# Kernel tuning notes

Measured on AMD Instinct MI355X. Metric: run time of the kernel, lower is better.

The kernel has to match this reference:

```python
import jax, jax.numpy as jnp
import numpy as np

STRIDES = (8, 16, 32)
NC = 80            # num_classes
BINS = 16          # dfl_bins
TOPK = 10          # tal_topk
TAL_ALPHA, TAL_BETA = 0.5, 6.0   # ultralytics TaskAlignedAssigner defaults
EPS = 1e-9
FOCAL_A, FOCAL_G = 0.25, 2.0
W_CLS, W_IOU, W_DFL = 0.5, 7.5, 1.5


def _make_grid(H, W, stride):
    ys, xs = jnp.meshgrid(jnp.arange(H, dtype=jnp.float32), jnp.arange(W, dtype=jnp.float32), indexing='ij')
    return jnp.stack([(xs + 0.5) * stride, (ys + 0.5) * stride], -1).reshape(H * W, 2)


def _flatten(p):
    # (B,C,H,W) -> cls (B,N,NC), dfl (B,N,4,BINS); channel layout = [4*BINS dfl | NC cls]
    B, C, H, W = p.shape
    p = p.transpose(0, 2, 3, 1).reshape(B, H * W, C)
    return p[..., 4 * BINS:], p[..., :4 * BINS].reshape(B, H * W, 4, BINS)


def _pairwise_iou(gt, pr):
    # gt (B,G,4), pr (B,N,4) -> iou (B,G,N)
    g = gt[:, :, None]
    p = pr[:, None]
    lt = jnp.maximum(g[..., :2], p[..., :2])
    rb = jnp.minimum(g[..., 2:], p[..., 2:])
    wh = jnp.clip(rb - lt, 0.0)
    inter = wh[..., 0] * wh[..., 1]
    ag = (g[..., 2] - g[..., 0]) * (g[..., 3] - g[..., 1])
    ap = jnp.clip(p[..., 2] - p[..., 0], 0.0) * jnp.clip(p[..., 3] - p[..., 1], 0.0)
    return inter / (ag + ap - inter + EPS)


def _ciou_loss(p, t):
    # elementwise CIoU loss, (...,4) xyxy -> (...)
    px1, py1, px2, py2 = p[..., 0], p[..., 1], p[..., 2], p[..., 3]
    tx1, ty1, tx2, ty2 = t[..., 0], t[..., 1], t[..., 2], t[..., 3]
    w1, h1 = px2 - px1, py2 - py1
    w2, h2 = tx2 - tx1, ty2 - ty1
    inter = jnp.clip(jnp.minimum(px2, tx2) - jnp.maximum(px1, tx1), 0.0) * \
            jnp.clip(jnp.minimum(py2, ty2) - jnp.maximum(py1, ty1), 0.0)
    union = w1 * h1 + w2 * h2 - inter + EPS
    iou = inter / union
    cw = jnp.maximum(px2, tx2) - jnp.minimum(px1, tx1)
    ch = jnp.maximum(py2, ty2) - jnp.minimum(py1, ty1)
    c2 = cw * cw + ch * ch + EPS
    rho2 = ((px1 + px2 - tx1 - tx2) ** 2 + (py1 + py2 - ty1 - ty2) ** 2) / 4.0
    v = (4.0 / np.pi ** 2) * (jnp.arctan(w2 / (h2 + EPS)) - jnp.arctan(w1 / (h1 + EPS))) ** 2
    alpha = jax.lax.stop_gradient(v / (v - iou + (1.0 + EPS)))
    return 1.0 - (iou - rho2 / c2 - v * alpha)


def _tal_assign(cls_prob, pred_boxes, grids, gt_bboxes, gt_labels):
    B, N, C = cls_prob.shape
    G = gt_bboxes.shape[1]
    idx = jnp.broadcast_to(gt_labels[:, None, :], (B, N, G))
    scores = jnp.take_along_axis(cls_prob, idx, axis=2).transpose(0, 2, 1)  # (B,G,N)
    overlaps = _pairwise_iou(gt_bboxes, pred_boxes)                          # (B,G,N)
    align = scores ** TAL_ALPHA * overlaps ** TAL_BETA
    x, y = grids[:, 0], grids[:, 1]
    in_gts = ((x[None, None] > gt_bboxes[..., 0:1]) & (x[None, None] < gt_bboxes[..., 2:3]) &
              (y[None, None] > gt_bboxes[..., 1:2]) & (y[None, None] < gt_bboxes[..., 3:4]))
    metric = jnp.where(in_gts, align, 0.0)
    vals, idxs = jax.lax.top_k(metric, TOPK)                                 # (B,G,TOPK)
    bi = jnp.arange(B)[:, None, None]
    gi = jnp.arange(G)[None, :, None]
    topk_mask = jnp.zeros((B, G, N), bool).at[bi, gi, idxs].set(vals > EPS)
    mask_pos = topk_mask & in_gts
    multi = mask_pos.sum(1) > 1                                              # (B,N)
    is_max = jnp.argmax(overlaps, 1)[:, None, :] == jnp.arange(G)[None, :, None]
    mask_pos = jnp.where(multi[:, None, :], is_max, mask_pos)
    fg = mask_pos.any(1)                                                     # (B,N)
    matched = jnp.argmax(mask_pos, 1)                                        # (B,N)
    mi = jnp.where(fg, matched, -1)
    b2 = jnp.arange(B)[:, None]
    tb = gt_bboxes[b2, matched]                                              # (B,N,4)
    tl = gt_labels[b2, matched]                                              # (B,N)
    mpf = mask_pos.astype(align.dtype)
    align_m = align * mpf
    ov_m = overlaps * mpf
    norm = (align_m * ov_m.max(-1, keepdims=True) / (align_m.max(-1, keepdims=True) + EPS)).max(1)
    ts = jax.nn.one_hot(tl, C, dtype=align.dtype) * norm[..., None] * fg[..., None]
    return ts, tb, fg, mi


def _dfl_targets(gt_bboxes, mi, fgf, grids, stride_map):
    # vectorized version of _make_dfl_targets: soft two-bin scatter per coord
    B, N = mi.shape
    b2 = jnp.arange(B)[:, None]
    boxes = gt_bboxes[b2, jnp.maximum(mi, 0)]                                # (B,N,4)
    cx, cy = grids[:, 0], grids[:, 1]
    d = jnp.stack([jnp.clip(cx - boxes[..., 0], 0.0), jnp.clip(cy - boxes[..., 1], 0.0),
                   jnp.clip(boxes[..., 2] - cx, 0.0), jnp.clip(boxes[..., 3] - cy, 0.0)], -1)
    d = jnp.clip(d / stride_map[None, :, None], 0.0, BINS - 1 - 1e-6)
    lo = jnp.floor(d)
    a = d - lo
    lo_i = lo.astype(jnp.int32)
    up_i = jnp.minimum(lo_i + 1, BINS - 1)
    td = jax.nn.one_hot(lo_i, BINS) * (1.0 - a)[..., None] + jax.nn.one_hot(up_i, BINS) * a[..., None]
    return td * fgf[..., None, None]                                         # (B,N,4,BINS)


def _focal_sum(logits, targets):
    logits = logits.reshape(-1, NC)
    targets = targets.reshape(-1, NC)
    p = jax.nn.sigmoid(logits)
    # stable BCE-with-logits
    ce = jnp.maximum(logits, 0.0) - logits * targets + jnp.log1p(jnp.exp(-jnp.abs(logits)))
    p_t = p * targets + (1.0 - p) * (1.0 - targets)
    a_t = targets * FOCAL_A + (1.0 - targets) * (1.0 - FOCAL_A)
    return (a_t * (1.0 - p_t) ** FOCAL_G * ce).sum()


def _loss(p0, p1, p2, gt_bboxes, gt_labels):
    cls_l, dfl_l, grid_l, str_l = [], [], [], []
    for p, s in zip((p0, p1, p2), STRIDES):
        c, d = _flatten(p)
        cls_l.append(c)
        dfl_l.append(d)
        H, W = p.shape[2], p.shape[3]
        grid_l.append(_make_grid(H, W, s))
        str_l.append(jnp.full((H * W,), float(s), jnp.float32))
    all_cls = jnp.concatenate(cls_l, 1)       # (B,N,NC)
    all_dfl = jnp.concatenate(dfl_l, 1)       # (B,N,4,BINS)
    grids = jnp.concatenate(grid_l, 0)        # (N,2)
    stride_map = jnp.concatenate(str_l, 0)    # (N,)
    # DFL decode: expectation over bins * stride -> ltrb -> xyxy
    dist = (jax.nn.softmax(all_dfl, -1) * jnp.arange(BINS, dtype=jnp.float32)).sum(-1) * stride_map[None, :, None]
    cx, cy = grids[:, 0], grids[:, 1]
    pred_boxes = jnp.stack([cx - dist[..., 0], cy - dist[..., 1], cx + dist[..., 2], cy + dist[..., 3]], -1)
    # assignment under stop_gradient (torch.no_grad in the original)
    cls_prob = jax.lax.stop_gradient(jax.nn.sigmoid(all_cls))
    pb_sg = jax.lax.stop_gradient(pred_boxes)
    ts, tb, fg, mi = _tal_assign(cls_prob, pb_sg, grids, gt_bboxes, gt_labels)
    ts = jax.lax.stop_gradient(ts)
    tb = jax.lax.stop_gradient(tb)
    fgf = fg.astype(jnp.float32)
    den = jnp.maximum(fg.sum(), 1).astype(jnp.float32)
    loss_iou = (_ciou_loss(pred_boxes, tb) * fgf).sum() / den
    tdfl = _dfl_targets(gt_bboxes, mi, fgf, grids, stride_map)
    loss_dfl = -(tdfl * jax.nn.log_softmax(all_dfl, -1)).sum() / den
    loss_cls = _focal_sum(all_cls, ts) / den
    return jnp.stack([W_IOU * loss_iou, W_DFL * loss_dfl, W_CLS * loss_cls])


def setup_inputs() -> dict:
    key = jax.random.key(0)
    ks = jax.random.split(key, 5)
    B, G = 16, 32
    p0 = jax.random.normal(ks[0], (B, 4 * BINS + NC, 80, 80), jnp.float32)
    p1 = jax.random.normal(ks[1], (B, 4 * BINS + NC, 40, 40), jnp.float32)
    p2 = jax.random.normal(ks[2], (B, 4 * BINS + NC, 20, 20), jnp.float32)
    u = jax.random.uniform(ks[3], (B, G, 4), jnp.float32)
    x1 = u[..., 0] * 560.0
    y1 = u[..., 1] * 560.0
    w = u[..., 2] * 140.0 + 20.0
    h = u[..., 3] * 140.0 + 20.0
    gt_bboxes = jnp.stack([x1, y1, jnp.minimum(x1 + w, 640.0), jnp.minimum(y1 + h, 640.0)], -1)
    gt_labels = jax.random.randint(ks[4], (B, G), 0, NC, jnp.int32)
    return {"p0": p0, "p1": p1, "p2": p2, "gt_bboxes": gt_bboxes, "gt_labels": gt_labels}


def reference(p0, p1, p2, gt_bboxes, gt_labels):
    return _loss(p0, p1, p2, gt_bboxes, gt_labels)
```

## Files before the change

### kernel.cpp

```cpp
#include <hip/hip_runtime.h>
#include <hip/hip_bf16.h>
#include <math.h>

#define NCC 80
#define BINS 16
#define NCH 144
#define NB 16
#define NG 32
#define NA 8400
#define HW0 6400
#define HW1 1600
#define HW2 400
#define TOPKK 10
#define EPSF 1e-9f
#define MAXC 832
#define MAXFG (NB*NG*TOPKK)
#define FGB (MAXFG/4)
#define NMASK (NB*NA)
#define FOCAL_BLOCKS 2625

__device__ __forceinline__ void anchor_geom(int n, float& cx, float& cy, float& st){
    if(n < HW0){ int y=n/80, x=n-y*80; st=8.f; cx=(x+0.5f)*8.f; cy=(y+0.5f)*8.f; }
    else if(n < HW0+HW1){ int m=n-HW0; int y=m/40, x=m-y*40; st=16.f; cx=(x+0.5f)*16.f; cy=(y+0.5f)*16.f; }
    else { int m=n-(HW0+HW1); int y=m/20, x=m-y*20; st=32.f; cx=(x+0.5f)*32.f; cy=(y+0.5f)*32.f; }
}

__device__ __forceinline__ const float* level_base(const float* p0, const float* p1, const float* p2,
                                                   int b, int n, int& m, int& hw){
    if(n < HW0){ m=n; hw=HW0; return p0 + (size_t)b*NCH*HW0; }
    if(n < HW0+HW1){ m=n-HW0; hw=HW1; return p1 + (size_t)b*NCH*HW1; }
    m=n-(HW0+HW1); hw=HW2; return p2 + (size_t)b*NCH*HW2;
}

__device__ __forceinline__ float iou_gp(float gx1,float gy1,float gx2,float gy2,
                                        float px1,float py1,float px2,float py2){
    float ltx = fmaxf(gx1, px1), lty = fmaxf(gy1, py1);
    float rbx = fminf(gx2, px2), rby = fminf(gy2, py2);
    float w = fmaxf(rbx-ltx, 0.f), h = fmaxf(rby-lty, 0.f);
    float inter = w*h;
    float ag = (gx2-gx1)*(gy2-gy1);
    float ap = fmaxf(px2-px1,0.f)*fmaxf(py2-py1,0.f);
    return inter/(ag+ap-inter+EPSF);
}

__device__ __forceinline__ float focal0(float x, float& p, float& ce0){
    float ax = fabsf(x);
    float e  = __expf(-ax);
    float r  = 1.f/(1.f+e);
    p   = (x >= 0.f) ? r : 1.f - r;
    ce0 = fmaxf(x,0.f) + __logf(1.f+e);
    return 0.75f*p*p*ce0;
}

__global__ __launch_bounds__(256) void k_decode(const float* __restrict__ p0, const float* __restrict__ p1,
                                                const float* __restrict__ p2, float* __restrict__ boxc,
                                                unsigned* __restrict__ maskg, float* __restrict__ amax,
                                                float* __restrict__ omax, int* __restrict__ cnt){
    int l = blockIdx.x*256 + threadIdx.x;
    maskg[l] = 0u;
    if(l < NB*NG){ amax[l] = 0.f; omax[l] = 0.f; }
    if(l == 0) *cnt = 0;
    int q = l % 2100;
    int j = (l / 2100) & 3;
    int b = l / 8400;
    const float* pl; int hw, m, n0, D; float st;
    if(q < 1600){ pl=p0; hw=HW0; m=4*q;        n0=m;         D=80; st=8.f; }
    else if(q < 2000){ pl=p1; hw=HW1; m=4*(q-1600); n0=HW0+m;     D=40; st=16.f; }
    else { pl=p2; hw=HW2; m=4*(q-2000); n0=HW0+HW1+m; D=20; st=32.f; }
    const float* ch = pl + ((size_t)b*NCH + j*BINS)*hw + m;
    float4 v[BINS];
    float4 mx = make_float4(-1e30f,-1e30f,-1e30f,-1e30f);
    #pragma unroll
    for(int k=0;k<BINS;k++){
        v[k] = *(const float4*)(ch + (size_t)k*hw);
        mx.x=fmaxf(mx.x,v[k].x); mx.y=fmaxf(mx.y,v[k].y);
        mx.z=fmaxf(mx.z,v[k].z); mx.w=fmaxf(mx.w,v[k].w);
    }
    float4 s = make_float4(0,0,0,0), acc = make_float4(0,0,0,0);
    #pragma unroll
    for(int k=0;k<BINS;k++){
        float fk=(float)k; float e;
        e=__expf(v[k].x-mx.x); s.x+=e; acc.x+=e*fk;
        e=__expf(v[k].y-mx.y); s.y+=e; acc.y+=e*fk;
        e=__expf(v[k].z-mx.z); s.z+=e; acc.z+=e*fk;
        e=__expf(v[k].w-mx.w); s.w+=e; acc.w+=e*fk;
    }
    float4 d = make_float4(acc.x/s.x*st, acc.y/s.y*st, acc.z/s.z*st, acc.w/s.w*st);
    int row = m / D, col = m - row*D;
    float cy = (row+0.5f)*st;
    float cx0=(col+0.5f)*st, cx1=(col+1.5f)*st, cx2=(col+2.5f)*st, cx3=(col+3.5f)*st;
    float4 o;
    if(j==0)      o = make_float4(cx0-d.x, cx1-d.y, cx2-d.z, cx3-d.w);
    else if(j==1) o = make_float4(cy -d.x, cy -d.y, cy -d.z, cy -d.w);
    else if(j==2) o = make_float4(cx0+d.x, cx1+d.y, cx2+d.z, cx3+d.w);
    else          o = make_float4(cy +d.x, cy +d.y, cy +d.z, cy +d.w);
    *(float4*)(boxc + (size_t)j*NB*NA + (size_t)b*NA + n0) = o;
}

__global__ __launch_bounds__(256) void k_assign(const float* __restrict__ p0, const float* __restrict__ p1,
                                                const float* __restrict__ p2, const float* __restrict__ boxc,
                                                const float* __restrict__ gtb, const int* __restrict__ gtl,
                                                unsigned* __restrict__ maskg){
    __shared__ float metric[MAXC];
    __shared__ int   candn[MAXC];
    __shared__ float rv[4]; __shared__ int ri[4];
    __shared__ float sbest; __shared__ int sbidx;
    int g = blockIdx.x, b = blockIdx.y, tid = threadIdx.x;
    const float* gb = gtb + ((size_t)b*NG + g)*4;
    float gx1=gb[0], gy1=gb[1], gx2=gb[2], gy2=gb[3];
    int label = gtl[b*NG+g];
    const float* bx1 = boxc + (size_t)b*NA;
    const float* by1 = bx1 + (size_t)NB*NA;
    const float* bx2 = by1 + (size_t)NB*NA;
    const float* by2 = bx2 + (size_t)NB*NA;

    int xs[3], ys[3], nxv[3], cc[3];
    #pragma unroll
    for(int lvl=0; lvl<3; lvl++){
        float s = (float)(8<<lvl); int D = 80>>lvl;
        int x0 = max(0, (int)floorf(gx1/s - 0.5f));
        int x1 = min(D-1, (int)ceilf (gx2/s - 0.5f));
        int y0 = max(0, (int)floorf(gy1/s - 0.5f));
        int y1 = min(D-1, (int)ceilf (gy2/s - 0.5f));
        xs[lvl]=x0; ys[lvl]=y0;
        nxv[lvl]=max(0, x1-x0+1);
        int nyv=max(0, y1-y0+1);
        cc[lvl]=nxv[lvl]*nyv;
    }
    int t0 = cc[0], t01 = cc[0]+cc[1], total = t01+cc[2];

    for(int c=tid; c<total; c+=256){
        int lvl, rel;
        if(c < t0){ lvl=0; rel=c; }
        else if(c < t01){ lvl=1; rel=c-t0; }
        else { lvl=2; rel=c-t01; }
        int yy = ys[lvl] + rel / nxv[lvl];
        int xx = xs[lvl] + rel % nxv[lvl];
        int D = 80>>lvl; float s = (float)(8<<lvl);
        int off = (lvl==0)?0:((lvl==1)?HW0:(HW0+HW1));
        int n = off + yy*D + xx;
        float cx = (xx+0.5f)*s, cy = (yy+0.5f)*s;
        float met = 0.f;
        if((cx>gx1)&&(cx<gx2)&&(cy>gy1)&&(cy<gy2)){
            float ov = iou_gp(gx1,gy1,gx2,gy2, bx1[n],by1[n],bx2[n],by2[n]);
            int m,hw; const float* base = level_base(p0,p1,p2,b,n,m,hw);
            float x = base[(size_t)(4*BINS+label)*hw + m];
            float sg = 1.f/(1.f+__expf(-x));
            float o2 = ov*ov;
            met = sqrtf(sg)*(o2*o2*o2);
        }
        metric[c] = met; candn[c] = n;
    }
    __syncthreads();

    for(int k=0;k<TOPKK;k++){
        float bv = -1.f; int bi = 0x7fffffff;
        for(int c=tid; c<total; c+=256){
            float v = metric[c];
            if(v > bv){ bv=v; bi=c; }
        }
        #pragma unroll
        for(int o=1; o<64; o<<=1){
            float ov = __shfl_xor(bv, o);
            int   oi = __shfl_xor(bi, o);
            if(ov > bv || (ov == bv && oi < bi)){ bv=ov; bi=oi; }
        }
        if((tid&63)==0){ rv[tid>>6]=bv; ri[tid>>6]=bi; }
        __syncthreads();
        if(tid==0){
            float fb=rv[0]; int fi=ri[0];
            #pragma unroll
            for(int w=1; w<4; w++)
                if(rv[w]>fb || (rv[w]==fb && ri[w]<fi)){ fb=rv[w]; fi=ri[w]; }
            sbest = fb; sbidx = fi;
            if(fb > EPSF){
                metric[fi] = -1.f;
                atomicOr(&maskg[(size_t)b*NA + candn[fi]], 1u<<g);
            }
        }
        __syncthreads();
        if(sbest <= EPSF) break;
    }
}

__global__ __launch_bounds__(256) void k_resolve(const float* __restrict__ p0, const float* __restrict__ p1,
                                                 const float* __restrict__ p2, const float* __restrict__ boxc,
                                                 const float* __restrict__ gtb, const int* __restrict__ gtl,
                                                 const unsigned* __restrict__ maskg,
                                                 float* __restrict__ amax, float* __restrict__ omax,
                                                 int* __restrict__ cnt, unsigned* __restrict__ fglist,
                                                 float* __restrict__ fgalign, float* __restrict__ fgx){
    __shared__ float sgt[NG*4];
    __shared__ int wcnt[4];
    __shared__ int sbase;
    int tid = threadIdx.x; int b = blockIdx.y;
    int wv = tid >> 6, lane = tid & 63;
    if(tid < NG*4) sgt[tid] = gtb[(size_t)b*NG*4 + tid];
    __syncthreads();
    int n = blockIdx.x*256 + tid;
    size_t bn = (size_t)b*NA + n;
    unsigned mask = (n < NA) ? maskg[bn] : 0u;
    bool fg = (mask != 0u);

    int match = 0; float ov = 0.f, av = 0.f, x = 0.f;
    if(fg){
        float px1 = boxc[bn], py1 = boxc[(size_t)NB*NA+bn],
              px2 = boxc[2*(size_t)NB*NA+bn], py2 = boxc[3*(size_t)NB*NA+bn];
        if(__popc(mask) > 1){
            float best = -1.f; int bi = 0;
            for(int g=0; g<NG; g++){
                float o = iou_gp(sgt[g*4],sgt[g*4+1],sgt[g*4+2],sgt[g*4+3],px1,py1,px2,py2);
                if(o > best){ best=o; bi=g; }
            }
            match = bi; ov = best;
        } else {
            match = __ffs(mask)-1;
            ov = iou_gp(sgt[match*4],sgt[match*4+1],sgt[match*4+2],sgt[match*4+3],px1,py1,px2,py2);
        }
        int label = gtl[b*NG+match];
        int m,hw; const float* base = level_base(p0,p1,p2,b,n,m,hw);
        x = base[(size_t)(4*BINS+label)*hw + m];
        float sg = 1.f/(1.f+__expf(-x));
        float ov2 = ov*ov;
        av = sqrtf(sg)*(ov2*ov2*ov2);
        atomicMax((int*)&amax[b*NG+match], __float_as_int(av));
        atomicMax((int*)&omax[b*NG+match], __float_as_int(ov));
    }
    unsigned long long bal = __ballot(fg);
    if(lane==0) wcnt[wv] = __popcll(bal);
    __syncthreads();
    if(tid==0){
        int tot = wcnt[0]+wcnt[1]+wcnt[2]+wcnt[3];
        sbase = tot ? atomicAdd(cnt, tot) : 0;
    }
    __syncthreads();
    if(fg){
        int woff = 0;
        for(int w=0; w<wv; w++) woff += wcnt[w];
        int before = __popcll(bal & ((1ull<<lane)-1ull));
        int pos = sbase + woff + before;
        fglist[pos]  = (unsigned)bn | ((unsigned)match << 18);
        fgalign[pos] = av;
        fgx[pos]     = x;
    }
}

__global__ __launch_bounds__(256) void k_fg(const float* __restrict__ p0, const float* __restrict__ p1,
                                            const float* __restrict__ p2, const float* __restrict__ boxc,
                                            const float* __restrict__ gtb,
                                            const float* __restrict__ amax, const float* __restrict__ omax,
                                            const int* __restrict__ cnt, const unsigned* __restrict__ fglist,
                                            const float* __restrict__ fgalign, const float* __restrict__ fgx,
                                            float* __restrict__ piou, float* __restrict__ pdfl,
                                            float* __restrict__ pfix){
    __shared__ float s4[12];
    int tid = threadIdx.x, wv = tid>>6, lane = tid&63;
    int i = blockIdx.x*4 + wv;
    float iou_l = 0.f, dfl_l = 0.f, fix_l = 0.f;
    if(i < *cnt){
        unsigned e = fglist[i];
        int bn = e & 0x3FFFF;
        int g  = e >> 18;
        int b  = bn / NA;
        int n  = bn - b*NA;
        float align = fgalign[i];
        float norm = align * omax[b*NG+g] / (amax[b*NG+g] + EPSF);
        const float* gb = gtb + ((size_t)b*NG+g)*4;
        float tx1=gb[0], ty1=gb[1], tx2=gb[2], ty2=gb[3];
        float px1 = boxc[bn], py1 = boxc[(size_t)NB*NA+bn],
              px2 = boxc[2*(size_t)NB*NA+bn], py2 = boxc[3*(size_t)NB*NA+bn];
        int m,hw; const float* base = level_base(p0,p1,p2,b,n,m,hw);
        float cx,cy,st; anchor_geom(n,cx,cy,st);
        int j = lane>>4, k = lane&15;
        float x = base[(size_t)lane*hw + m];
        float dt = (j==0)?(cx-tx1):((j==1)?(cy-ty1):((j==2)?(tx2-cx):(ty2-cy)));
        float d = fminf(fmaxf(dt,0.f)/st, 14.999999f);
        float lo = floorf(d); float a = d-lo;
        int li = (int)lo; int ui = min(li+1, BINS-1);
        float mx = x;
        #pragma unroll
        for(int o=1;o<16;o<<=1) mx = fmaxf(mx, __shfl_xor(mx,o));
        float ex = __expf(x-mx);
        float se = ex;
        #pragma unroll
        for(int o=1;o<16;o<<=1) se += __shfl_xor(se,o);
        float lse = mx + __logf(se);
        float coef = ((k==li)?(1.f-a):0.f) + ((k==ui)?a:0.f);
        dfl_l = -coef*(x-lse);
        if(lane==0){
            float w1=px2-px1, h1=py2-py1, w2=tx2-tx1, h2=ty2-ty1;
            float inter = fmaxf(fminf(px2,tx2)-fmaxf(px1,tx1),0.f) *
                          fmaxf(fminf(py2,ty2)-fmaxf(py1,ty1),0.f);
            float uni = w1*h1 + w2*h2 - inter + EPSF;
            float iou = inter/uni;
            float cwd = fmaxf(px2,tx2)-fminf(px1,tx1);
            float chd = fmaxf(py2,ty2)-fminf(py1,ty1);
            float c2 = cwd*cwd + chd*chd + EPSF;
            float dx = px1+px2-tx1-tx2, dy = py1+py2-ty1-ty2;
            float rho2 = (dx*dx + dy*dy)*0.25f;
            float dv = atanf(w2/(h2+EPSF)) - atanf(w1/(h1+EPSF));
            float v = 0.40528473456935108577f*dv*dv;
            float alpha = v/(v - iou + 1.f + EPSF);
            iou_l = 1.f - (iou - rho2/c2 - v*alpha);
            float fx = fgx[i];
            float p, ce0;
            float f0 = focal0(fx, p, ce0);
            float tv = norm;
            float cet = ce0 - fx*tv;
            float pt = p*tv + (1.f-p)*(1.f-tv);
            float at = 0.25f*tv + 0.75f*(1.f-tv);
            float om = 1.f-pt;
            fix_l = at*om*om*cet - f0;
        }
    }
    #pragma unroll
    for(int o=32; o; o>>=1){
        iou_l += __shfl_down(iou_l, o);
        dfl_l += __shfl_down(dfl_l, o);
        fix_l += __shfl_down(fix_l, o);
    }
    if(lane==0){ s4[wv]=iou_l; s4[4+wv]=dfl_l; s4[8+wv]=fix_l; }
    __syncthreads();
    if(tid==0){
        piou[blockIdx.x] = s4[0]+s4[1]+s4[2]+s4[3];
        pdfl[blockIdx.x] = s4[4]+s4[5]+s4[6]+s4[7];
        pfix[blockIdx.x] = s4[8]+s4[9]+s4[10]+s4[11];
    }
}

__global__ __launch_bounds__(256) void k_focal(const float* __restrict__ p0, const float* __restrict__ p1,
                                               const float* __restrict__ p2, float* __restrict__ pcls){
    __shared__ float s4[4];
    int tid = threadIdx.x;
    int t = blockIdx.x*256 + tid;
    float acc = 0.f;
    #pragma unroll
    for(int it=0; it<4; ++it){
        int i4 = t + it*672000;
        const float4* src;
        if(i4 < 2048000){
            int b = i4 / 128000; int r = i4 - b*128000;
            src = (const float4*)(p0 + (size_t)b*921600 + 409600) + r;
        } else if(i4 < 2560000){
            int j = i4 - 2048000; int b = j / 32000; int r = j - b*32000;
            src = (const float4*)(p1 + (size_t)b*230400 + 102400) + r;
        } else {
            int j = i4 - 2560000; int b = j / 8000; int r = j - b*8000;
            src = (const float4*)(p2 + (size_t)b*57600 + 25600) + r;
        }
        float4 x4 = *src;
        float p, c;
        acc += focal0(x4.x, p, c);
        acc += focal0(x4.y, p, c);
        acc += focal0(x4.z, p, c);
        acc += focal0(x4.w, p, c);
    }
    #pragma unroll
    for(int off=32; off; off>>=1) acc += __shfl_down(acc, off);
    if((tid&63)==0) s4[tid>>6] = acc;
    __syncthreads();
    if(tid==0) pcls[blockIdx.x] = s4[0]+s4[1]+s4[2]+s4[3];
}

__global__ __launch_bounds__(256) void k_final(const float* __restrict__ pcls, const float* __restrict__ piou,
                                               const float* __restrict__ pdfl, const float* __restrict__ pfix,
                                               const int* __restrict__ cnt, float* __restrict__ out){
    __shared__ float sa[4], sb[4], sc[4], sd[4];
    int tid = threadIdx.x;
    float a = 0.f, b3 = 0.f, c3 = 0.f, d3 = 0.f;
    for(int i=tid; i<FOCAL_BLOCKS; i+=256) a += pcls[i];
    for(int i=tid; i<FGB; i+=256){ b3 += piou[i]; c3 += pdfl[i]; d3 += pfix[i]; }
    #pragma unroll
    for(int off=32; off; off>>=1){
        a  += __shfl_down(a,  off);
        b3 += __shfl_down(b3, off);
        c3 += __shfl_down(c3, off);
        d3 += __shfl_down(d3, off);
    }
    if((tid&63)==0){ int w=tid>>6; sa[w]=a; sb[w]=b3; sc[w]=c3; sd[w]=d3; }
    __syncthreads();
    if(tid==0){
        float A=sa[0]+sa[1]+sa[2]+sa[3], B=sb[0]+sb[1]+sb[2]+sb[3];
        float C=sc[0]+sc[1]+sc[2]+sc[3], D=sd[0]+sd[1]+sd[2]+sd[3];
        int c = *cnt;
        float den = (float)(c > 1 ? c : 1);
        out[0] = 7.5f * B / den;
        out[1] = 1.5f * C / den;
        out[2] = 0.5f * (A + D) / den;
    }
}

extern "C" void kernel_launch(void* const* d_in, const int* in_sizes, int n_in,
                              void* d_out, int out_size, void* d_ws, size_t ws_size,
                              hipStream_t stream) {
    (void)in_sizes; (void)n_in; (void)out_size; (void)ws_size;
    const float* p0  = (const float*)d_in[0];
    const float* p1  = (const float*)d_in[1];
    const float* p2  = (const float*)d_in[2];
    const float* gtb = (const float*)d_in[3];
    const int*   gtl = (const int*)d_in[4];
    float* out = (float*)d_out;

    char* ws = (char*)d_ws;
    const size_t COMP = (size_t)NB*NA*4;
    size_t off = 0;
    int*      cnt    = (int*)     (ws + off); off += 16;
    float*    amax   = (float*)   (ws + off); off += NB*NG*4;
    float*    omax   = (float*)   (ws + off); off += NB*NG*4;
    unsigned* maskg  = (unsigned*)(ws + off); off += COMP;
    float*    boxc   = (float*)   (ws + off); off += 4*COMP;
    unsigned* fglist = (unsigned*)(ws + off); off += MAXFG*4;
    float*    fgalign= (float*)   (ws + off); off += MAXFG*4;
    float*    fgx    = (float*)   (ws + off); off += MAXFG*4;
    float*    pcls   = (float*)   (ws + off); off += FOCAL_BLOCKS*4;
    float*    piou   = (float*)   (ws + off); off += FGB*4;
    float*    pdfl   = (float*)   (ws + off); off += FGB*4;
    float*    pfix   = (float*)   (ws + off); off += FGB*4;

    dim3 blk(256);
    k_decode <<<525,             blk, 0, stream>>>(p0,p1,p2, boxc, maskg, amax, omax, cnt);
    k_assign <<<dim3(NG,NB),     blk, 0, stream>>>(p0,p1,p2, boxc, gtb, gtl, maskg);
    k_resolve<<<dim3(33,NB),     blk, 0, stream>>>(p0,p1,p2, boxc, gtb, gtl, maskg,
                                                   amax, omax, cnt, fglist, fgalign, fgx);
    k_fg     <<<FGB,             blk, 0, stream>>>(p0,p1,p2, boxc, gtb, amax, omax,
                                                   cnt, fglist, fgalign, fgx, piou, pdfl, pfix);
    k_focal  <<<FOCAL_BLOCKS,    blk, 0, stream>>>(p0,p1,p2, pcls);
    k_final  <<<1,               blk, 0, stream>>>(pcls, piou, pdfl, pfix, cnt, out);
}
```

Before: 151.6 us.

## Merge decode with focal pass and fold final reduction into fg kernel

The DFL decode and the background focal-loss sum now run as one launch whose block index selects the role, so the two independent bandwidth-bound passes share the GPU instead of running back to back. The separate final reduction kernel is removed. The last foreground block, found with an atomic counter and a thread fence, now does the global reduction. Together this cuts the launch count from six to four and removes idle tails between kernels. The cost is a workspace counter that must be reset every call and a serial final reduction done by a single block.

```diff
diff --git a/kernel.cpp b/kernel.cpp
--- a/kernel.cpp
+++ b/kernel.cpp
@@ -17,7 +17,9 @@
 #define MAXFG (NB*NG*TOPKK)
 #define FGB (MAXFG/4)
 #define NMASK (NB*NA)
+#define DEC_BLOCKS 525
 #define FOCAL_BLOCKS 2625
+#define MAIN_BLOCKS (DEC_BLOCKS + FOCAL_BLOCKS)
 
 __device__ __forceinline__ void anchor_geom(int n, float& cx, float& cy, float& st){
     if(n < HW0){ int y=n/80, x=n-y*80; st=8.f; cx=(x+0.5f)*8.f; cy=(y+0.5f)*8.f; }
@@ -52,49 +54,84 @@
     return 0.75f*p*p*ce0;
 }
 
-__global__ __launch_bounds__(256) void k_decode(const float* __restrict__ p0, const float* __restrict__ p1,
-                                                const float* __restrict__ p2, float* __restrict__ boxc,
-                                                unsigned* __restrict__ maskg, float* __restrict__ amax,
-                                                float* __restrict__ omax, int* __restrict__ cnt){
-    int l = blockIdx.x*256 + threadIdx.x;
-    maskg[l] = 0u;
-    if(l < NB*NG){ amax[l] = 0.f; omax[l] = 0.f; }
-    if(l == 0) *cnt = 0;
-    int q = l % 2100;
-    int j = (l / 2100) & 3;
-    int b = l / 8400;
-    const float* pl; int hw, m, n0, D; float st;
-    if(q < 1600){ pl=p0; hw=HW0; m=4*q;        n0=m;         D=80; st=8.f; }
-    else if(q < 2000){ pl=p1; hw=HW1; m=4*(q-1600); n0=HW0+m;     D=40; st=16.f; }
-    else { pl=p2; hw=HW2; m=4*(q-2000); n0=HW0+HW1+m; D=20; st=32.f; }
-    const float* ch = pl + ((size_t)b*NCH + j*BINS)*hw + m;
-    float4 v[BINS];
-    float4 mx = make_float4(-1e30f,-1e30f,-1e30f,-1e30f);
-    #pragma unroll
-    for(int k=0;k<BINS;k++){
-        v[k] = *(const float4*)(ch + (size_t)k*hw);
-        mx.x=fmaxf(mx.x,v[k].x); mx.y=fmaxf(mx.y,v[k].y);
-        mx.z=fmaxf(mx.z,v[k].z); mx.w=fmaxf(mx.w,v[k].w);
-    }
-    float4 s = make_float4(0,0,0,0), acc = make_float4(0,0,0,0);
-    #pragma unroll
-    for(int k=0;k<BINS;k++){
-        float fk=(float)k; float e;
-        e=__expf(v[k].x-mx.x); s.x+=e; acc.x+=e*fk;
-        e=__expf(v[k].y-mx.y); s.y+=e; acc.y+=e*fk;
-        e=__expf(v[k].z-mx.z); s.z+=e; acc.z+=e*fk;
-        e=__expf(v[k].w-mx.w); s.w+=e; acc.w+=e*fk;
-    }
-    float4 d = make_float4(acc.x/s.x*st, acc.y/s.y*st, acc.z/s.z*st, acc.w/s.w*st);
-    int row = m / D, col = m - row*D;
-    float cy = (row+0.5f)*st;
-    float cx0=(col+0.5f)*st, cx1=(col+1.5f)*st, cx2=(col+2.5f)*st, cx3=(col+3.5f)*st;
-    float4 o;
-    if(j==0)      o = make_float4(cx0-d.x, cx1-d.y, cx2-d.z, cx3-d.w);
-    else if(j==1) o = make_float4(cy -d.x, cy -d.y, cy -d.z, cy -d.w);
-    else if(j==2) o = make_float4(cx0+d.x, cx1+d.y, cx2+d.z, cx3+d.w);
-    else          o = make_float4(cy +d.x, cy +d.y, cy +d.z, cy +d.w);
-    *(float4*)(boxc + (size_t)j*NB*NA + (size_t)b*NA + n0) = o;
+__global__ __launch_bounds__(256) void k_main(const float* __restrict__ p0, const float* __restrict__ p1,
+                                              const float* __restrict__ p2, float* __restrict__ boxc,
+                                              unsigned* __restrict__ maskg, float* __restrict__ amax,
+                                              float* __restrict__ omax, int* __restrict__ cnt,
+                                              int* __restrict__ done, float* __restrict__ pcls){
+    int tid = threadIdx.x;
+    if(blockIdx.x < DEC_BLOCKS){
+        int l = blockIdx.x*256 + tid;
+        maskg[l] = 0u;
+        if(l < NB*NG){ amax[l] = 0.f; omax[l] = 0.f; }
+        if(l == 0){ *cnt = 0; *done = 0; }
+        int q = l % 2100;
+        int j = (l / 2100) & 3;
+        int b = l / 8400;
+        const float* pl; int hw, m, n0, D; float st;
+        if(q < 1600){ pl=p0; hw=HW0; m=4*q;        n0=m;         D=80; st=8.f; }
+        else if(q < 2000){ pl=p1; hw=HW1; m=4*(q-1600); n0=HW0+m;     D=40; st=16.f; }
+        else { pl=p2; hw=HW2; m=4*(q-2000); n0=HW0+HW1+m; D=20; st=32.f; }
+        const float* ch = pl + ((size_t)b*NCH + j*BINS)*hw + m;
+        float4 v[BINS];
+        float4 mx = make_float4(-1e30f,-1e30f,-1e30f,-1e30f);
+        #pragma unroll
+        for(int k=0;k<BINS;k++){
+            v[k] = *(const float4*)(ch + (size_t)k*hw);
+            mx.x=fmaxf(mx.x,v[k].x); mx.y=fmaxf(mx.y,v[k].y);
+            mx.z=fmaxf(mx.z,v[k].z); mx.w=fmaxf(mx.w,v[k].w);
+        }
+        float4 s = make_float4(0,0,0,0), acc = make_float4(0,0,0,0);
+        #pragma unroll
+        for(int k=0;k<BINS;k++){
+            float fk=(float)k; float e;
+            e=__expf(v[k].x-mx.x); s.x+=e; acc.x+=e*fk;
+            e=__expf(v[k].y-mx.y); s.y+=e; acc.y+=e*fk;
+            e=__expf(v[k].z-mx.z); s.z+=e; acc.z+=e*fk;
+            e=__expf(v[k].w-mx.w); s.w+=e; acc.w+=e*fk;
+        }
+        float4 d = make_float4(acc.x/s.x*st, acc.y/s.y*st, acc.z/s.z*st, acc.w/s.w*st);
+        int row = m / D, col = m - row*D;
+        float cy = (row+0.5f)*st;
+        float cx0=(col+0.5f)*st, cx1=(col+1.5f)*st, cx2=(col+2.5f)*st, cx3=(col+3.5f)*st;
+        float4 o;
+        if(j==0)      o = make_float4(cx0-d.x, cx1-d.y, cx2-d.z, cx3-d.w);
+        else if(j==1) o = make_float4(cy -d.x, cy -d.y, cy -d.z, cy -d.w);
+        else if(j==2) o = make_float4(cx0+d.x, cx1+d.y, cx2+d.z, cx3+d.w);
+        else          o = make_float4(cy +d.x, cy +d.y, cy +d.z, cy +d.w);
+        *(float4*)(boxc + (size_t)j*NB*NA + (size_t)b*NA + n0) = o;
+    } else {
+        __shared__ float s4[4];
+        int blk = blockIdx.x - DEC_BLOCKS;
+        int t = blk*256 + tid;
+        float acc = 0.f;
+        #pragma unroll
+        for(int it=0; it<4; ++it){
+            int i4 = t + it*672000;
+            const float4* src;
+            if(i4 < 2048000){
+                int b = i4 / 128000; int r = i4 - b*128000;
+                src = (const float4*)(p0 + (size_t)b*921600 + 409600) + r;
+            } else if(i4 < 2560000){
+                int j = i4 - 2048000; int b = j / 32000; int r = j - b*32000;
+                src = (const float4*)(p1 + (size_t)b*230400 + 102400) + r;
+            } else {
+                int j = i4 - 2560000; int b = j / 8000; int r = j - b*8000;
+                src = (const float4*)(p2 + (size_t)b*57600 + 25600) + r;
+            }
+            float4 x4 = *src;
+            float p, c;
+            acc += focal0(x4.x, p, c);
+            acc += focal0(x4.y, p, c);
+            acc += focal0(x4.z, p, c);
+            acc += focal0(x4.w, p, c);
+        }
+        #pragma unroll
+        for(int off=32; off; off>>=1) acc += __shfl_down(acc, off);
+        if((tid&63)==0) s4[tid>>6] = acc;
+        __syncthreads();
+        if(tid==0) pcls[blk] = s4[0]+s4[1]+s4[2]+s4[3];
+    }
 }
 
 __global__ __launch_bounds__(256) void k_assign(const float* __restrict__ p0, const float* __restrict__ p1,
@@ -104,7 +141,7 @@
     __shared__ float metric[MAXC];
     __shared__ int   candn[MAXC];
     __shared__ float rv[4]; __shared__ int ri[4];
-    __shared__ float sbest; __shared__ int sbidx;
+    __shared__ float sbest;
     int g = blockIdx.x, b = blockIdx.y, tid = threadIdx.x;
     const float* gb = gtb + ((size_t)b*NG + g)*4;
     float gx1=gb[0], gy1=gb[1], gx2=gb[2], gy2=gb[3];
@@ -172,7 +209,7 @@
             #pragma unroll
             for(int w=1; w<4; w++)
                 if(rv[w]>fb || (rv[w]==fb && ri[w]<fi)){ fb=rv[w]; fi=ri[w]; }
-            sbest = fb; sbidx = fi;
+            sbest = fb;
             if(fb > EPSF){
                 metric[fi] = -1.f;
                 atomicOr(&maskg[(size_t)b*NA + candn[fi]], 1u<<g);
@@ -245,15 +282,18 @@
     }
 }
 
-__global__ __launch_bounds__(256) void k_fg(const float* __restrict__ p0, const float* __restrict__ p1,
-                                            const float* __restrict__ p2, const float* __restrict__ boxc,
-                                            const float* __restrict__ gtb,
-                                            const float* __restrict__ amax, const float* __restrict__ omax,
-                                            const int* __restrict__ cnt, const unsigned* __restrict__ fglist,
-                                            const float* __restrict__ fgalign, const float* __restrict__ fgx,
-                                            float* __restrict__ piou, float* __restrict__ pdfl,
-                                            float* __restrict__ pfix){
+__global__ __launch_bounds__(256) void k_fgfin(const float* __restrict__ p0, const float* __restrict__ p1,
+                                               const float* __restrict__ p2, const float* __restrict__ boxc,
+                                               const float* __restrict__ gtb,
+                                               const float* __restrict__ amax, const float* __restrict__ omax,
+                                               const int* __restrict__ cnt, const unsigned* __restrict__ fglist,
+                                               const float* __restrict__ fgalign, const float* __restrict__ fgx,
+                                               float* __restrict__ piou, float* __restrict__ pdfl,
+                                               float* __restrict__ pfix, const float* __restrict__ pcls,
+                                               int* __restrict__ done, float* __restrict__ out){
     __shared__ float s4[12];
+    __shared__ float sa[4], sb[4], sc[4], sd[4];
+    __shared__ int slast;
     int tid = threadIdx.x, wv = tid>>6, lane = tid&63;
     int i = blockIdx.x*4 + wv;
     float iou_l = 0.f, dfl_l = 0.f, fix_l = 0.f;
@@ -325,68 +365,35 @@
         piou[blockIdx.x] = s4[0]+s4[1]+s4[2]+s4[3];
         pdfl[blockIdx.x] = s4[4]+s4[5]+s4[6]+s4[7];
         pfix[blockIdx.x] = s4[8]+s4[9]+s4[10]+s4[11];
-    }
-}
-
-__global__ __launch_bounds__(256) void k_focal(const float* __restrict__ p0, const float* __restrict__ p1,
-                                               const float* __restrict__ p2, float* __restrict__ pcls){
-    __shared__ float s4[4];
-    int tid = threadIdx.x;
-    int t = blockIdx.x*256 + tid;
-    float acc = 0.f;
+        __threadfence();
+        int old = atomicAdd(done, 1);
+        slast = (old == FGB-1) ? 1 : 0;
+    }
+    __syncthreads();
+    if(!slast) return;
+    __threadfence();
+    float A = 0.f, B = 0.f, C = 0.f, D = 0.f;
+    for(int t=tid; t<FOCAL_BLOCKS; t+=256) A += pcls[t];
+    for(int t=tid; t<FGB; t+=256){ B += piou[t]; C += pdfl[t]; D += pfix[t]; }
     #pragma unroll
-    for(int it=0; it<4; ++it){
-        int i4 = t + it*672000;
-        const float4* src;
-        if(i4 < 2048000){
-            int b = i4 / 128000; int r = i4 - b*128000;
-            src = (const float4*)(p0 + (size_t)b*921600 + 409600) + r;
-        } else if(i4 < 2560000){
-            int j = i4 - 2048000; int b = j / 32000; int r = j - b*32000;
-            src = (const float4*)(p1 + (size_t)b*230400 + 102400) + r;
-        } else {
-            int j = i4 - 2560000; int b = j / 8000; int r = j - b*8000;
-            src = (const float4*)(p2 + (size_t)b*57600 + 25600) + r;
-        }
-        float4 x4 = *src;
-        float p, c;
-        acc += focal0(x4.x, p, c);
-        acc += focal0(x4.y, p, c);
-        acc += focal0(x4.z, p, c);
-        acc += focal0(x4.w, p, c);
-    }
-    #pragma unroll
-    for(int off=32; off; off>>=1) acc += __shfl_down(acc, off);
-    if((tid&63)==0) s4[tid>>6] = acc;
-    __syncthreads();
-    if(tid==0) pcls[blockIdx.x] = s4[0]+s4[1]+s4[2]+s4[3];
-}
-
-__global__ __launch_bounds__(256) void k_final(const float* __restrict__ pcls, const float* __restrict__ piou,
-                                               const float* __restrict__ pdfl, const float* __restrict__ pfix,
-                                               const int* __restrict__ cnt, float* __restrict__ out){
-    __shared__ float sa[4], sb[4], sc[4], sd[4];
-    int tid = threadIdx.x;
-    float a = 0.f, b3 = 0.f, c3 = 0.f, d3 = 0.f;
-    for(int i=tid; i<FOCAL_BLOCKS; i+=256) a += pcls[i];
-    for(int i=tid; i<FGB; i+=256){ b3 += piou[i]; c3 += pdfl[i]; d3 += pfix[i]; }
-    #pragma unroll
-    for(int off=32; off; off>>=1){
-        a  += __shfl_down(a,  off);
-        b3 += __shfl_down(b3, off);
-        c3 += __shfl_down(c3, off);
-        d3 += __shfl_down(d3, off);
-    }
-    if((tid&63)==0){ int w=tid>>6; sa[w]=a; sb[w]=b3; sc[w]=c3; sd[w]=d3; }
+    for(int o=32; o; o>>=1){
+        A += __shfl_down(A, o);
+        B += __shfl_down(B, o);
+        C += __shfl_down(C, o);
+        D += __shfl_down(D, o);
+    }
+    if(lane==0){ sa[wv]=A; sb[wv]=B; sc[wv]=C; sd[wv]=D; }
     __syncthreads();
     if(tid==0){
-        float A=sa[0]+sa[1]+sa[2]+sa[3], B=sb[0]+sb[1]+sb[2]+sb[3];
-        float C=sc[0]+sc[1]+sc[2]+sc[3], D=sd[0]+sd[1]+sd[2]+sd[3];
+        float a = sa[0]+sa[1]+sa[2]+sa[3];
+        float bb = sb[0]+sb[1]+sb[2]+sb[3];
+        float cc2 = sc[0]+sc[1]+sc[2]+sc[3];
+        float dd = sd[0]+sd[1]+sd[2]+sd[3];
         int c = *cnt;
         float den = (float)(c > 1 ? c : 1);
-        out[0] = 7.5f * B / den;
-        out[1] = 1.5f * C / den;
-        out[2] = 0.5f * (A + D) / den;
+        out[0] = 7.5f * bb / den;
+        out[1] = 1.5f * cc2 / den;
+        out[2] = 0.5f * (a + dd) / den;
     }
 }
 
@@ -405,6 +412,7 @@
     const size_t COMP = (size_t)NB*NA*4;
     size_t off = 0;
     int*      cnt    = (int*)     (ws + off); off += 16;
+    int*      done   = (int*)     (ws + off); off += 16;
     float*    amax   = (float*)   (ws + off); off += NB*NG*4;
     float*    omax   = (float*)   (ws + off); off += NB*NG*4;
     unsigned* maskg  = (unsigned*)(ws + off); off += COMP;
@@ -418,12 +426,11 @@
     float*    pfix   = (float*)   (ws + off); off += FGB*4;
 
     dim3 blk(256);
-    k_decode <<<525,             blk, 0, stream>>>(p0,p1,p2, boxc, maskg, amax, omax, cnt);
-    k_assign <<<dim3(NG,NB),     blk, 0, stream>>>(p0,p1,p2, boxc, gtb, gtl, maskg);
-    k_resolve<<<dim3(33,NB),     blk, 0, stream>>>(p0,p1,p2, boxc, gtb, gtl, maskg,
-                                                   amax, omax, cnt, fglist, fgalign, fgx);
-    k_fg     <<<FGB,             blk, 0, stream>>>(p0,p1,p2, boxc, gtb, amax, omax,
-                                                   cnt, fglist, fgalign, fgx, piou, pdfl, pfix);
-    k_focal  <<<FOCAL_BLOCKS,    blk, 0, stream>>>(p0,p1,p2, pcls);
-    k_final  <<<1,               blk, 0, stream>>>(pcls, piou, pdfl, pfix, cnt, out);
-}
+    k_main   <<<MAIN_BLOCKS,   blk, 0, stream>>>(p0,p1,p2, boxc, maskg, amax, omax, cnt, done, pcls);
+    k_assign <<<dim3(NG,NB),   blk, 0, stream>>>(p0,p1,p2, boxc, gtb, gtl, maskg);
+    k_resolve<<<dim3(33,NB),   blk, 0, stream>>>(p0,p1,p2, boxc, gtb, gtl, maskg,
+                                                 amax, omax, cnt, fglist, fgalign, fgx);
+    k_fgfin  <<<FGB,           blk, 0, stream>>>(p0,p1,p2, boxc, gtb, amax, omax,
+                                                 cnt, fglist, fgalign, fgx, piou, pdfl, pfix,
+                                                 pcls, done, out);
+}
```

Result: slower. 171.5 us (+13.1%).
